# Kernel optimization log

Hardware: AMD Instinct MI355X
Metric: run time of the kernel (lower is better)

The kernel has to match this reference:

```python
import jax, jax.numpy as jnp
import numpy as np

B, H, S, D = 8, 16, 512, 512  # note: module's final matmul requires D == S


def setup_inputs() -> dict:
    key = jax.random.key(0)
    kq, kk, kv = jax.random.split(key, 3)
    q = jax.random.normal(kq, (B, H, S, D), dtype=jnp.float32)
    k = jax.random.normal(kk, (B, H, S, D), dtype=jnp.float32)
    v = jax.random.normal(kv, (B, H, S, D), dtype=jnp.float32)
    return {"q": q, "k": k, "v": v}


def reference(q, k, v):
    # scaled = (q @ k^T) / sqrt(d_k); mask path is unreachable in the original
    scale = 1.0 / jnp.sqrt(jnp.asarray(q.shape[-1], dtype=q.dtype))
    scores = jax.nn.softmax(scale * jnp.einsum('bhsd,bhtd->bhst', q, k), axis=-1)
    # NOTE: faithful to the original's nonstandard scores @ v^T (not scores @ v)
    out = jnp.einsum('bhst,bhdt->bhsd', scores, v)  # == scores @ v.swapaxes(-2,-1)
    return out
```

## Files before the change

### kernel.cpp

```cpp
#include <hip/hip_runtime.h>
#include <hip/hip_bf16.h>


typedef __attribute__((ext_vector_type(4))) float floatx4;
typedef __attribute__((ext_vector_type(8))) short shortx8;

#define SEQ 512
#define DIM 512
#define MQ   64
#define NTH 512
#define KCH  32
#define LDA 520
#define LDB  40

__device__ __forceinline__ unsigned short f2bf(float f) {
  union { __hip_bfloat16 b; unsigned short u; } cv;
  cv.b = __float2bfloat16(f);
  return cv.u;
}

__device__ __forceinline__ uint2 cvt4(float4 f) {
  union { __hip_bfloat162 b; unsigned int u; } lo, hi;
  lo.b = __float22bfloat162_rn(make_float2(f.x, f.y));
  hi.b = __float22bfloat162_rn(make_float2(f.z, f.w));
  uint2 r; r.x = lo.u; r.y = hi.u;
  return r;
}

__global__ __launch_bounds__(NTH, 1)
void sdpa_kernel(const float* __restrict__ q, const float* __restrict__ k,
                 const float* __restrict__ v, float* __restrict__ out) {
  __shared__ unsigned short smA[MQ * LDA];
  __shared__ unsigned short smB[SEQ * LDB];
  __shared__ float red[MQ][4];

  const int tid  = threadIdx.x;
  const int lane = tid & 63;
  const int wid  = tid >> 6;
  const int strip = wid >> 1;
  const int half  = wid & 1;
  const int l15  = lane & 15;
  const int quad = lane >> 4;

  const int id = blockIdx.x;
  const int c  = id & 7;
  const int g  = id >> 3;
  const int qtile = g & 7;
  const int head  = ((g >> 3) << 3) | c;

  const size_t hb = (size_t)head * (SEQ * DIM);
  const float* qh = q + hb + (size_t)qtile * MQ * DIM;
  const float* kh = k + hb;
  const float* vh = v + hb;
  float*       oh = out + hb + (size_t)qtile * MQ * DIM;

  const float scale = 0.044194173824159216f;

  #pragma unroll
  for (int i = 0; i < 16; ++i) {
    int flat = i * NTH + tid;
    int row  = flat >> 7;
    int c4   = flat & 127;
    float4 f = *(const float4*)(qh + row * DIM + (c4 << 2));
    f.x *= scale; f.y *= scale; f.z *= scale; f.w *= scale;
    *(uint2*)(&smA[row * LDA + (c4 << 2)]) = cvt4(f);
  }

  floatx4 acc[16];
  #pragma unroll
  for (int i = 0; i < 16; ++i) acc[i] = (floatx4)(0.0f);

  for (int kc = 0; kc < 16; ++kc) {
    #pragma unroll
    for (int i = 0; i < 8; ++i) {
      int flat = i * NTH + tid;
      int row  = flat >> 3;
      int c4   = flat & 7;
      float4 f = *(const float4*)(kh + row * DIM + kc * KCH + (c4 << 2));
      *(uint2*)(&smB[row * LDB + (c4 << 2)]) = cvt4(f);
    }
    __syncthreads();
    shortx8 a = *(const shortx8*)(&smA[(strip * 16 + l15) * LDA + kc * KCH + quad * 8]);
    #pragma unroll
    for (int ct = 0; ct < 16; ++ct) {
      shortx8 b = *(const shortx8*)(&smB[(half * 256 + ct * 16 + l15) * LDB + quad * 8]);
      acc[ct] = __builtin_amdgcn_mfma_f32_16x16x32_bf16(a, b, acc[ct], 0, 0, 0);
    }
    __syncthreads();
  }

  float mx[4], sm[4];
  #pragma unroll
  for (int r = 0; r < 4; ++r) mx[r] = -1e30f;
  #pragma unroll
  for (int ct = 0; ct < 16; ++ct)
    #pragma unroll
    for (int r = 0; r < 4; ++r) mx[r] = fmaxf(mx[r], acc[ct][r]);
  #pragma unroll
  for (int off = 8; off >= 1; off >>= 1)
    #pragma unroll
    for (int r = 0; r < 4; ++r) mx[r] = fmaxf(mx[r], __shfl_xor(mx[r], off, 16));

  const int row0 = strip * 16 + quad * 4;
  if (l15 == 0) {
    #pragma unroll
    for (int r = 0; r < 4; ++r) red[row0 + r][half] = mx[r];
  }
  __syncthreads();
  #pragma unroll
  for (int r = 0; r < 4; ++r) {
    mx[r] = fmaxf(red[row0 + r][0], red[row0 + r][1]);
    sm[r] = 0.0f;
  }
  #pragma unroll
  for (int ct = 0; ct < 16; ++ct)
    #pragma unroll
    for (int r = 0; r < 4; ++r) {
      float e = __expf(acc[ct][r] - mx[r]);
      acc[ct][r] = e;
      sm[r] += e;
    }
  #pragma unroll
  for (int off = 8; off >= 1; off >>= 1)
    #pragma unroll
    for (int r = 0; r < 4; ++r) sm[r] += __shfl_xor(sm[r], off, 16);
  if (l15 == 0) {
    #pragma unroll
    for (int r = 0; r < 4; ++r) red[row0 + r][2 + half] = sm[r];
  }
  __syncthreads();
  float inv[4];
  #pragma unroll
  for (int r = 0; r < 4; ++r) inv[r] = 1.0f / (red[row0 + r][2] + red[row0 + r][3]);

  #pragma unroll
  for (int ct = 0; ct < 16; ++ct) {
    int t = half * 256 + ct * 16 + l15;
    #pragma unroll
    for (int r = 0; r < 4; ++r) {
      smA[(row0 + r) * LDA + t] = f2bf(acc[ct][r] * inv[r]);
    }
  }

  #pragma unroll
  for (int i = 0; i < 16; ++i) acc[i] = (floatx4)(0.0f);

  for (int tc = 0; tc < 16; ++tc) {
    #pragma unroll
    for (int i = 0; i < 8; ++i) {
      int flat = i * NTH + tid;
      int row  = flat >> 3;
      int c4   = flat & 7;
      float4 f = *(const float4*)(vh + row * DIM + tc * KCH + (c4 << 2));
      *(uint2*)(&smB[row * LDB + (c4 << 2)]) = cvt4(f);
    }
    __syncthreads();
    shortx8 a = *(const shortx8*)(&smA[(strip * 16 + l15) * LDA + tc * KCH + quad * 8]);
    #pragma unroll
    for (int dt = 0; dt < 16; ++dt) {
      shortx8 b = *(const shortx8*)(&smB[(half * 256 + dt * 16 + l15) * LDB + quad * 8]);
      acc[dt] = __builtin_amdgcn_mfma_f32_16x16x32_bf16(a, b, acc[dt], 0, 0, 0);
    }
    __syncthreads();
  }

  #pragma unroll
  for (int dt = 0; dt < 16; ++dt) {
    int col = half * 256 + dt * 16 + l15;
    #pragma unroll
    for (int r = 0; r < 4; ++r) {
      oh[(row0 + r) * DIM + col] = acc[dt][r];
    }
  }
}

extern "C" void kernel_launch(void* const* d_in, const int* in_sizes, int n_in,
                              void* d_out, int out_size, void* d_ws, size_t ws_size,
                              hipStream_t stream) {
  const float* q = (const float*)d_in[0];
  const float* k = (const float*)d_in[1];
  const float* v = (const float*)d_in[2];
  float* out = (float*)d_out;
  (void)in_sizes; (void)n_in; (void)out_size; (void)d_ws; (void)ws_size;
  sdpa_kernel<<<dim3(8 * 16 * (SEQ / MQ)), dim3(NTH), 0, stream>>>(q, k, v, out);
}
```

Measured before the change: 597.0 us.

## Double-buffer K/V tiles with register prefetch and XOR-swizzled shared layout

New measurement: 549.8 us. 1.09x faster.

```diff
diff --git a/kernel.cpp b/kernel.cpp
--- a/kernel.cpp
+++ b/kernel.cpp
@@ -11,7 +11,7 @@
 #define NTH 512
 #define KCH  32
 #define LDA 520
-#define LDB  40
+#define LDBS 32
 
 __device__ __forceinline__ unsigned short f2bf(float f) {
   union { __hip_bfloat16 b; unsigned short u; } cv;
@@ -31,7 +31,7 @@
 void sdpa_kernel(const float* __restrict__ q, const float* __restrict__ k,
                  const float* __restrict__ v, float* __restrict__ out) {
   __shared__ unsigned short smA[MQ * LDA];
-  __shared__ unsigned short smB[SEQ * LDB];
+  __shared__ unsigned short smB[2][SEQ * LDBS];
   __shared__ float red[MQ][4];
 
   const int tid  = threadIdx.x;
@@ -43,10 +43,10 @@
   const int quad = lane >> 4;
 
   const int id = blockIdx.x;
-  const int c  = id & 7;
+  const int cx = id & 7;
   const int g  = id >> 3;
   const int qtile = g & 7;
-  const int head  = ((g >> 3) << 3) | c;
+  const int head  = ((g >> 3) << 3) | cx;
 
   const size_t hb = (size_t)head * (SEQ * DIM);
   const float* qh = q + hb + (size_t)qtile * MQ * DIM;
@@ -56,37 +56,60 @@
 
   const float scale = 0.044194173824159216f;
 
-  #pragma unroll
-  for (int i = 0; i < 16; ++i) {
-    int flat = i * NTH + tid;
-    int row  = flat >> 7;
-    int c4   = flat & 127;
-    float4 f = *(const float4*)(qh + row * DIM + (c4 << 2));
-    f.x *= scale; f.y *= scale; f.z *= scale; f.w *= scale;
-    *(uint2*)(&smA[row * LDA + (c4 << 2)]) = cvt4(f);
-  }
+  const int r0 = tid >> 3;
+  const int c4 = tid & 7;
+  const int sldx = r0 * LDBS + ((c4 ^ (r0 & 6)) << 2);
+
+  float4 rv[8];
+
+  #pragma unroll
+  for (int i = 0; i < 8; ++i)
+    rv[i] = *(const float4*)(kh + (size_t)(i * 64 + r0) * DIM + (c4 << 2));
+
+  {
+    const int qc  = tid & 127;
+    const int qr0 = tid >> 7;
+    #pragma unroll
+    for (int i = 0; i < 16; ++i) {
+      int row = i * 4 + qr0;
+      float4 f = *(const float4*)(qh + (size_t)row * DIM + (qc << 2));
+      f.x *= scale; f.y *= scale; f.z *= scale; f.w *= scale;
+      *(uint2*)(&smA[row * LDA + (qc << 2)]) = cvt4(f);
+    }
+  }
+
+  #pragma unroll
+  for (int i = 0; i < 8; ++i)
+    *(uint2*)(&smB[0][i * 64 * LDBS + sldx]) = cvt4(rv[i]);
+  __syncthreads();
 
   floatx4 acc[16];
   #pragma unroll
   for (int i = 0; i < 16; ++i) acc[i] = (floatx4)(0.0f);
 
+  const int arow = (strip * 16 + l15) * LDA + quad * 8;
+  const int bu = (((quad << 1) ^ (l15 & 6)) << 2);
+
+  int cur = 0;
   for (int kc = 0; kc < 16; ++kc) {
-    #pragma unroll
-    for (int i = 0; i < 8; ++i) {
-      int flat = i * NTH + tid;
-      int row  = flat >> 3;
-      int c4   = flat & 7;
-      float4 f = *(const float4*)(kh + row * DIM + kc * KCH + (c4 << 2));
-      *(uint2*)(&smB[row * LDB + (c4 << 2)]) = cvt4(f);
-    }
+    const float* src = (kc < 15) ? (kh + (kc + 1) * KCH) : vh;
+    #pragma unroll
+    for (int i = 0; i < 8; ++i)
+      rv[i] = *(const float4*)(src + (size_t)(i * 64 + r0) * DIM + (c4 << 2));
+
+    shortx8 a = *(const shortx8*)(&smA[arow + kc * KCH]);
+    #pragma unroll
+    for (int ct = 0; ct < 16; ++ct) {
+      int brow = half * 256 + ct * 16 + l15;
+      shortx8 b = *(const shortx8*)(&smB[cur][brow * LDBS + bu]);
+      acc[ct] = __builtin_amdgcn_mfma_f32_16x16x32_bf16(a, b, acc[ct], 0, 0, 0);
+    }
+    __builtin_amdgcn_sched_barrier(0);
+    #pragma unroll
+    for (int i = 0; i < 8; ++i)
+      *(uint2*)(&smB[cur ^ 1][i * 64 * LDBS + sldx]) = cvt4(rv[i]);
     __syncthreads();
-    shortx8 a = *(const shortx8*)(&smA[(strip * 16 + l15) * LDA + kc * KCH + quad * 8]);
-    #pragma unroll
-    for (int ct = 0; ct < 16; ++ct) {
-      shortx8 b = *(const shortx8*)(&smB[(half * 256 + ct * 16 + l15) * LDB + quad * 8]);
-      acc[ct] = __builtin_amdgcn_mfma_f32_16x16x32_bf16(a, b, acc[ct], 0, 0, 0);
-    }
-    __syncthreads();
+    cur ^= 1;
   }
 
   float mx[4], sm[4];
@@ -141,27 +164,33 @@
       smA[(row0 + r) * LDA + t] = f2bf(acc[ct][r] * inv[r]);
     }
   }
+  __syncthreads();
 
   #pragma unroll
   for (int i = 0; i < 16; ++i) acc[i] = (floatx4)(0.0f);
 
   for (int tc = 0; tc < 16; ++tc) {
-    #pragma unroll
-    for (int i = 0; i < 8; ++i) {
-      int flat = i * NTH + tid;
-      int row  = flat >> 3;
-      int c4   = flat & 7;
-      float4 f = *(const float4*)(vh + row * DIM + tc * KCH + (c4 << 2));
-      *(uint2*)(&smB[row * LDB + (c4 << 2)]) = cvt4(f);
-    }
-    __syncthreads();
-    shortx8 a = *(const shortx8*)(&smA[(strip * 16 + l15) * LDA + tc * KCH + quad * 8]);
+    if (tc < 15) {
+      #pragma unroll
+      for (int i = 0; i < 8; ++i)
+        rv[i] = *(const float4*)(vh + (size_t)(i * 64 + r0) * DIM
+                                 + (tc + 1) * KCH + (c4 << 2));
+    }
+    shortx8 a = *(const shortx8*)(&smA[arow + tc * KCH]);
     #pragma unroll
     for (int dt = 0; dt < 16; ++dt) {
-      shortx8 b = *(const shortx8*)(&smB[(half * 256 + dt * 16 + l15) * LDB + quad * 8]);
+      int brow = half * 256 + dt * 16 + l15;
+      shortx8 b = *(const shortx8*)(&smB[cur][brow * LDBS + bu]);
       acc[dt] = __builtin_amdgcn_mfma_f32_16x16x32_bf16(a, b, acc[dt], 0, 0, 0);
     }
-    __syncthreads();
+    if (tc < 15) {
+      __builtin_amdgcn_sched_barrier(0);
+      #pragma unroll
+      for (int i = 0; i < 8; ++i)
+        *(uint2*)(&smB[cur ^ 1][i * 64 * LDBS + sldx]) = cvt4(rv[i]);
+      __syncthreads();
+      cur ^= 1;
+    }
   }
 
   #pragma unroll
```
